# Kernel optimization log

Hardware: AMD Instinct MI355X
Metric: run time of the kernel (lower is better)

The kernel has to match this reference:

```python
import jax, jax.numpy as jnp
import numpy as np

D_MODEL = 1024
D_FF = 4 * D_MODEL
NUM_EXPERTS = 8
TOP_K = 2
BATCH, SEQ = 2, 2048


def setup_inputs() -> dict:
    key = jax.random.key(0)
    ks = jax.random.split(key, 6)
    s_in = 1.0 / np.sqrt(D_MODEL)
    s_ff = 1.0 / np.sqrt(D_FF)
    x = jax.random.normal(ks[0], (BATCH, SEQ, D_MODEL), dtype=jnp.float32)
    Wg = jax.random.uniform(ks[1], (D_MODEL, NUM_EXPERTS), minval=-s_in, maxval=s_in, dtype=jnp.float32)
    W1 = jax.random.uniform(ks[2], (NUM_EXPERTS, D_MODEL, D_FF), minval=-s_in, maxval=s_in, dtype=jnp.float32)
    b1 = jax.random.uniform(ks[3], (NUM_EXPERTS, D_FF), minval=-s_in, maxval=s_in, dtype=jnp.float32)
    W2 = jax.random.uniform(ks[4], (NUM_EXPERTS, D_FF, D_MODEL), minval=-s_ff, maxval=s_ff, dtype=jnp.float32)
    b2 = jax.random.uniform(ks[5], (NUM_EXPERTS, D_MODEL), minval=-s_ff, maxval=s_ff, dtype=jnp.float32)
    return {"x": x, "Wg": Wg, "W1": W1, "b1": b1, "W2": W2, "b2": b2}


def reference(x, Wg, W1, b1, W2, b2):
    B, S, D = x.shape
    x_flat = x.reshape(-1, D)                      # [T, D]
    gate_logits = x_flat @ Wg                      # [T, E] (eval mode: no noise)
    gate_probs = jax.nn.softmax(gate_logits, axis=-1)
    top_v, top_i = jax.lax.top_k(gate_probs, TOP_K)            # [T, k]
    top_v = top_v / (jnp.sum(top_v, axis=-1, keepdims=True) + 1e-8)
    out = jnp.zeros_like(x_flat)
    for e in range(NUM_EXPERTS):
        # combine weight for expert e: sum of normalized top-k probs routed here
        w_e = jnp.sum(jnp.where(top_i == e, top_v, 0.0), axis=-1)   # [T]
        h = jax.nn.gelu(x_flat @ W1[e] + b1[e], approximate=False)  # [T, F]
        y = h @ W2[e] + b2[e]                                       # [T, D]
        out = out + w_e[:, None] * y
    return out.reshape(B, S, D)
```

## Files before the change

### kernel.cpp

```cpp
#include <hip/hip_runtime.h>
#include <math.h>

typedef __attribute__((ext_vector_type(8))) short short8;
typedef __attribute__((ext_vector_type(4))) float f32x4;
typedef unsigned short u16;

#define NT 4096
#define DM 1024
#define DF 4096
#define NE 8
#define HROWS 9216

static __device__ __forceinline__ u16 f2bf(float f) {
  union { float f; unsigned u; } v; v.f = f;
  return (u16)((v.u + 0x7fffu + ((v.u >> 16) & 1u)) >> 16);
}

static __device__ __forceinline__ void gload16(const void* g, void* l) {
  __builtin_amdgcn_global_load_lds((const __attribute__((address_space(1))) void*)g,
                                   (__attribute__((address_space(3))) void*)l, 16, 0, 0);
}

__global__ __launch_bounds__(256) void gate_k(const float* __restrict__ x,
                                              const float* __restrict__ Wg,
                                              int* __restrict__ te,
                                              float* __restrict__ tw) {
  int t = blockIdx.x * 4 + (threadIdx.x >> 6);
  int l = threadIdx.x & 63;
  float a0=0,a1=0,a2=0,a3=0,a4=0,a5=0,a6=0,a7=0;
  const float* xr = x + (size_t)t * DM;
  for (int k = l; k < DM; k += 64) {
    float xv = xr[k];
    const float4* wp = (const float4*)(Wg + k * 8);
    float4 w0 = wp[0], w1 = wp[1];
    a0 += xv * w0.x; a1 += xv * w0.y; a2 += xv * w0.z; a3 += xv * w0.w;
    a4 += xv * w1.x; a5 += xv * w1.y; a6 += xv * w1.z; a7 += xv * w1.w;
  }
#pragma unroll
  for (int s = 32; s >= 1; s >>= 1) {
    a0 += __shfl_down(a0, s); a1 += __shfl_down(a1, s);
    a2 += __shfl_down(a2, s); a3 += __shfl_down(a3, s);
    a4 += __shfl_down(a4, s); a5 += __shfl_down(a5, s);
    a6 += __shfl_down(a6, s); a7 += __shfl_down(a7, s);
  }
  if (l == 0) {
    float lg[8] = {a0,a1,a2,a3,a4,a5,a6,a7};
    float m = lg[0];
#pragma unroll
    for (int e = 1; e < 8; ++e) m = fmaxf(m, lg[e]);
    float p[8], s = 0.f;
#pragma unroll
    for (int e = 0; e < 8; ++e) { p[e] = expf(lg[e] - m); s += p[e]; }
#pragma unroll
    for (int e = 0; e < 8; ++e) p[e] /= s;
    int i0 = 0; float v0 = p[0];
#pragma unroll
    for (int e = 1; e < 8; ++e) if (p[e] > v0) { v0 = p[e]; i0 = e; }
    int i1 = -1; float v1 = -1.f;
#pragma unroll
    for (int e = 0; e < 8; ++e) {
      if (e == i0) continue;
      if (p[e] > v1) { v1 = p[e]; i1 = e; }
    }
    float norm = v0 + v1 + 1e-8f;
    te[t*2]   = i0; te[t*2+1] = i1;
    tw[t*2]   = v0 / norm; tw[t*2+1] = v1 / norm;
  }
}

__global__ __launch_bounds__(256) void route_k(const int* __restrict__ te,
                                               const float* __restrict__ tw,
                                               int* __restrict__ meta,
                                               int* __restrict__ lt,
                                               float* __restrict__ lw) {
  int i = blockIdx.x * 256 + threadIdx.x;
  if (i >= NT * 2) return;
  int e = te[i];
  float w = tw[i];
  int pos = atomicAdd(&meta[e], 1);
  lt[e * NT + pos] = i;
  lw[e * NT + pos] = w;
}

__global__ __launch_bounds__(256) void finalize_k(int* __restrict__ meta,
                                                  int* __restrict__ lt,
                                                  float* __restrict__ lw) {
  __shared__ int s_cnt[8], s_pc[8];
  if (threadIdx.x == 0) {
    int base = 0;
    for (int e = 0; e < 8; ++e) {
      int c = meta[e];
      int pc = (c + 127) & ~127;
      s_cnt[e] = c; s_pc[e] = pc;
      meta[8 + e] = pc;
      meta[16 + e] = base;
      base += pc;
    }
  }
  __syncthreads();
  for (int e = 0; e < 8; ++e) {
    int c = s_cnt[e], pc = s_pc[e];
    for (int i = c + (int)threadIdx.x; i < pc; i += 256) {
      lt[e * NT + i] = 2 * NT;
      lw[e * NT + i] = 0.f;
    }
  }
}

__global__ __launch_bounds__(256) void prep_x(const float* __restrict__ x, u16* __restrict__ xbf) {
  size_t i = (size_t)blockIdx.x * 256 + threadIdx.x;
  const float4* p = (const float4*)(x + i * 8);
  float4 a = p[0], b = p[1];
  short8 o = { (short)f2bf(a.x), (short)f2bf(a.y), (short)f2bf(a.z), (short)f2bf(a.w),
               (short)f2bf(b.x), (short)f2bf(b.y), (short)f2bf(b.z), (short)f2bf(b.w) };
  *(short8*)(xbf + i * 8) = o;
}

__global__ __launch_bounds__(256) void prep_wT(const float* __restrict__ in,
                                               u16* __restrict__ out, int K, int N) {
  const int e = blockIdx.z;
  const int n0 = blockIdx.x * 64, k0 = blockIdx.y * 64;
  const float* ie = in + (size_t)e * K * N;
  u16* oe = out + (size_t)e * K * N;
  __shared__ u16 t[64 * 72];
  const int tid = threadIdx.x;
  const int kr = tid >> 4, nq = (tid & 15) * 4;
#pragma unroll
  for (int it = 0; it < 4; ++it) {
    int k = it * 16 + kr;
    float4 v = *(const float4*)(ie + (size_t)(k0 + k) * N + n0 + nq);
    t[(nq + 0) * 72 + k] = f2bf(v.x);
    t[(nq + 1) * 72 + k] = f2bf(v.y);
    t[(nq + 2) * 72 + k] = f2bf(v.z);
    t[(nq + 3) * 72 + k] = f2bf(v.w);
  }
  __syncthreads();
#pragma unroll
  for (int it = 0; it < 2; ++it) {
    int idx = it * 256 + tid;
    int n = idx >> 3, kc = idx & 7;
    short8 v = *(const short8*)&t[n * 72 + kc * 8];
    *(short8*)(oe + (size_t)(n0 + n) * K + k0 + kc * 8) = v;
  }
}

__global__ __launch_bounds__(256) void ffn1_k(const u16* __restrict__ xbf,
                                              const u16* __restrict__ W1T,
                                              const float* __restrict__ b1,
                                              const int* __restrict__ lt,
                                              const int* __restrict__ meta,
                                              u16* __restrict__ H) {
  const int e = blockIdx.z, mt = blockIdx.y, nt = blockIdx.x;
  const int pc = meta[8 + e];
  if (mt * 128 >= pc) return;
  const int rbase = meta[16 + e];

  __shared__ u16 As[128 * 32];
  __shared__ u16 Bs[128 * 32];

  const int tid = threadIdx.x, lane = tid & 63, wv = tid >> 6;
  const int wm = wv >> 1, wn = wv & 1, l15 = lane & 15, l4 = lane >> 4;

  const u16* pa[2]; const u16* pb[2]; u16* la[2]; u16* lb[2];
#pragma unroll
  for (int it = 0; it < 2; ++it) {
    int idx = it * 256 + tid;
    int r = idx >> 2, s = idx & 3;
    int kg = s ^ ((r >> 1) & 3);
    int tok = lt[e * NT + mt * 128 + r] >> 1;
    if (tok >= NT) tok = 0;
    pa[it] = xbf + (size_t)tok * DM + kg * 8;
    pb[it] = W1T + ((size_t)e * DF + nt * 128 + r) * DM + kg * 8;
    la[it] = As + (it * 256 + wv * 64) * 8;
    lb[it] = Bs + (it * 256 + wv * 64) * 8;
  }

  int aoff[4], boff[4];
#pragma unroll
  for (int i = 0; i < 4; ++i) {
    int ra = wm * 64 + i * 16 + l15;
    aoff[i] = ra * 32 + (l4 ^ ((ra >> 1) & 3)) * 8;
    int rb = wn * 64 + i * 16 + l15;
    boff[i] = rb * 32 + (l4 ^ ((rb >> 1) & 3)) * 8;
  }

  f32x4 acc[4][4];
#pragma unroll
  for (int mi = 0; mi < 4; ++mi)
#pragma unroll
    for (int ni = 0; ni < 4; ++ni) acc[mi][ni] = 0.f;

  for (int ks = 0; ks < DM / 32; ++ks) {
    __syncthreads();
    gload16(pa[0], la[0]); gload16(pa[1], la[1]);
    gload16(pb[0], lb[0]); gload16(pb[1], lb[1]);
    pa[0] += 32; pa[1] += 32; pb[0] += 32; pb[1] += 32;
    __syncthreads();

    short8 af[4], bf_[4];
#pragma unroll
    for (int i = 0; i < 4; ++i) {
      af[i]  = *(const short8*)&As[aoff[i]];
      bf_[i] = *(const short8*)&Bs[boff[i]];
    }
#pragma unroll
    for (int mi = 0; mi < 4; ++mi)
#pragma unroll
      for (int ni = 0; ni < 4; ++ni)
        acc[mi][ni] = __builtin_amdgcn_mfma_f32_16x16x32_bf16(af[mi], bf_[ni], acc[mi][ni], 0, 0, 0);
  }

  const size_t hrow0 = (size_t)rbase + mt * 128;
#pragma unroll
  for (int mi = 0; mi < 4; ++mi) {
#pragma unroll
    for (int ni = 0; ni < 4; ++ni) {
      int gn = nt * 128 + wn * 64 + ni * 16 + l15;
      float bias = b1[e * DF + gn];
      int r0 = wm * 64 + mi * 16 + l4 * 4;
#pragma unroll
      for (int j = 0; j < 4; ++j) {
        float v = acc[mi][ni][j] + bias;
        v = 0.5f * v * (1.0f + erff(v * 0.70710678118654752f));
        H[(hrow0 + r0 + j) * DF + gn] = f2bf(v);
      }
    }
  }
}

template <bool USEY>
__global__ __launch_bounds__(256) void ffn2_k(const u16* __restrict__ H,
                                              const u16* __restrict__ W2T,
                                              const float* __restrict__ b2,
                                              const int* __restrict__ lt,
                                              const float* __restrict__ lw,
                                              const int* __restrict__ meta,
                                              float* __restrict__ Y,
                                              float* __restrict__ out) {
  const int e = blockIdx.z, mt = blockIdx.y, nt = blockIdx.x;
  const int pc = meta[8 + e];
  if (mt * 128 >= pc) return;
  const int rbase = meta[16 + e];

  __shared__ u16 As[128 * 32];
  __shared__ u16 Bs[128 * 32];
  __shared__ int s_ts[128];
  __shared__ float s_w[128];

  const int tid = threadIdx.x, lane = tid & 63, wv = tid >> 6;
  const int wm = wv >> 1, wn = wv & 1, l15 = lane & 15, l4 = lane >> 4;

  if (tid < 128) {
    s_ts[tid] = lt[e * NT + mt * 128 + tid];
    s_w[tid]  = lw[e * NT + mt * 128 + tid];
  }

  const u16* pa[2]; const u16* pb[2]; u16* la[2]; u16* lb[2];
#pragma unroll
  for (int it = 0; it < 2; ++it) {
    int idx = it * 256 + tid;
    int r = idx >> 2, s = idx & 3;
    int kg = s ^ ((r >> 1) & 3);
    pa[it] = H + ((size_t)rbase + mt * 128 + r) * DF + kg * 8;
    pb[it] = W2T + ((size_t)e * DM + nt * 128 + r) * DF + kg * 8;
    la[it] = As + (it * 256 + wv * 64) * 8;
    lb[it] = Bs + (it * 256 + wv * 64) * 8;
  }

  int aoff[4], boff[4];
#pragma unroll
  for (int i = 0; i < 4; ++i) {
    int ra = wm * 64 + i * 16 + l15;
    aoff[i] = ra * 32 + (l4 ^ ((ra >> 1) & 3)) * 8;
    int rb = wn * 64 + i * 16 + l15;
    boff[i] = rb * 32 + (l4 ^ ((rb >> 1) & 3)) * 8;
  }

  f32x4 acc[4][4];
#pragma unroll
  for (int mi = 0; mi < 4; ++mi)
#pragma unroll
    for (int ni = 0; ni < 4; ++ni) acc[mi][ni] = 0.f;

  for (int ks = 0; ks < DF / 32; ++ks) {
    __syncthreads();
    gload16(pa[0], la[0]); gload16(pa[1], la[1]);
    gload16(pb[0], lb[0]); gload16(pb[1], lb[1]);
    pa[0] += 32; pa[1] += 32; pb[0] += 32; pb[1] += 32;
    __syncthreads();

    short8 af[4], bf_[4];
#pragma unroll
    for (int i = 0; i < 4; ++i) {
      af[i]  = *(const short8*)&As[aoff[i]];
      bf_[i] = *(const short8*)&Bs[boff[i]];
    }
#pragma unroll
    for (int mi = 0; mi < 4; ++mi)
#pragma unroll
      for (int ni = 0; ni < 4; ++ni)
        acc[mi][ni] = __builtin_amdgcn_mfma_f32_16x16x32_bf16(af[mi], bf_[ni], acc[mi][ni], 0, 0, 0);
  }

#pragma unroll
  for (int mi = 0; mi < 4; ++mi) {
#pragma unroll
    for (int ni = 0; ni < 4; ++ni) {
      int gn = nt * 128 + wn * 64 + ni * 16 + l15;
      float bias = b2[e * DM + gn];
      int r0 = wm * 64 + mi * 16 + l4 * 4;
#pragma unroll
      for (int j = 0; j < 4; ++j) {
        int r = r0 + j;
        float w = s_w[r];
        int ts = s_ts[r];
        float v = w * (acc[mi][ni][j] + bias);
        if (USEY) {
          Y[(size_t)ts * DM + gn] = v;
        } else {
          int tok = ts >> 1;
          if (tok >= NT) tok = 0;
          atomicAdd(out + (size_t)tok * DM + gn, v);
        }
      }
    }
  }
}

__global__ __launch_bounds__(256) void combine_k(const float* __restrict__ Y,
                                                 float* __restrict__ out) {
  size_t i4 = (size_t)blockIdx.x * 256 + threadIdx.x;
  size_t t = i4 >> 8;
  int c4 = (int)(i4 & 255) * 4;
  const float4 a = *(const float4*)(Y + (2 * t) * DM + c4);
  const float4 b = *(const float4*)(Y + (2 * t + 1) * DM + c4);
  float4 o = { a.x + b.x, a.y + b.y, a.z + b.z, a.w + b.w };
  *(float4*)(out + t * DM + c4) = o;
}

extern "C" void kernel_launch(void* const* d_in, const int* in_sizes, int n_in,
                              void* d_out, int out_size, void* d_ws, size_t ws_size,
                              hipStream_t stream) {
  const float* x  = (const float*)d_in[0];
  const float* Wg = (const float*)d_in[1];
  const float* W1 = (const float*)d_in[2];
  const float* b1 = (const float*)d_in[3];
  const float* W2 = (const float*)d_in[4];
  const float* b2 = (const float*)d_in[5];
  float* out = (float*)d_out;

  char* ws = (char*)d_ws;
  size_t o = 0;
  auto take = [&](size_t sz) { size_t p = o; o = (o + sz + 1023) & ~(size_t)1023; return p; };

  int*   meta = (int*)(ws + take(1024));
  int*   te   = (int*)(ws + take((size_t)NT * 2 * 4));
  float* tw   = (float*)(ws + take((size_t)NT * 2 * 4));
  int*   lt   = (int*)(ws + take((size_t)NE * NT * 4));
  float* lw   = (float*)(ws + take((size_t)NE * NT * 4));
  u16*   xbf  = (u16*)(ws + take((size_t)NT * DM * 2));
  u16*   W1T  = (u16*)(ws + take((size_t)NE * DM * DF * 2));
  u16*   H    = (u16*)(ws + take((size_t)HROWS * DF * 2));
  size_t needB = o;
  size_t needA = needB + ((size_t)NE * DM * DF * 2 + 1024) + ((size_t)(2 * NT + 8) * DM * 4 + 1024);

  bool pathA = (ws_size >= needA);
  u16*   W2T;
  float* Y = nullptr;
  if (pathA) {
    W2T = (u16*)(ws + take((size_t)NE * DM * DF * 2));
    Y   = (float*)(ws + take((size_t)(2 * NT + 8) * DM * 4));
  } else {
    W2T = W1T;
  }

  hipMemsetAsync(meta, 0, 1024, stream);
  if (!pathA) hipMemsetAsync(out, 0, (size_t)NT * DM * 4, stream);

  gate_k<<<NT / 4, 256, 0, stream>>>(x, Wg, te, tw);
  route_k<<<(NT * 2) / 256, 256, 0, stream>>>(te, tw, meta, lt, lw);
  finalize_k<<<1, 256, 0, stream>>>(meta, lt, lw);
  prep_x<<<(NT * DM / 8) / 256, 256, 0, stream>>>(x, xbf);
  prep_wT<<<dim3(DF / 64, DM / 64, NE), 256, 0, stream>>>(W1, W1T, DM, DF);
  if (pathA)
    prep_wT<<<dim3(DM / 64, DF / 64, NE), 256, 0, stream>>>(W2, W2T, DF, DM);

  ffn1_k<<<dim3(DF / 128, NT / 128, NE), 256, 0, stream>>>(xbf, W1T, b1, lt, meta, H);

  if (!pathA)
    prep_wT<<<dim3(DM / 64, DF / 64, NE), 256, 0, stream>>>(W2, W2T, DF, DM);

  if (pathA) {
    ffn2_k<true><<<dim3(DM / 128, NT / 128, NE), 256, 0, stream>>>(H, W2T, b2, lt, lw, meta, Y, out);
    combine_k<<<NT, 256, 0, stream>>>(Y, out);
  } else {
    ffn2_k<false><<<dim3(DM / 128, NT / 128, NE), 256, 0, stream>>>(H, W2T, b2, lt, lw, meta, Y, out);
  }
}
```

Measured before the change: 395.3 us.

## Double-buffer LDS in expert GEMMs, compact tile list, split-K for FFN2

Both expert GEMM kernels now use two LDS buffers. The next K-slice is loaded with global_load_lds while MFMAs run on the current one, and each step ends with one waitcnt and barrier instead of two barriers. The grid is built from a compact list of (expert, m-tile) pairs written by finalize_k, so empty blocks are not launched. When workspace allows, FFN2 splits K into two halves that write separate Y buffers, which combine_k sums. This raises occupancy for the small FFN2 grid at the cost of double LDS use and an extra Y buffer to write and read.

```diff
diff --git a/kernel.cpp b/kernel.cpp
--- a/kernel.cpp
+++ b/kernel.cpp
@@ -10,6 +10,8 @@
 #define DF 4096
 #define NE 8
 #define HROWS 9216
+#define TIT 72
+#define YROWS (2 * NT + 8)
 
 static __device__ __forceinline__ u16 f2bf(float f) {
   union { float f; unsigned u; } v; v.f = f;
@@ -87,7 +89,7 @@
                                                   float* __restrict__ lw) {
   __shared__ int s_cnt[8], s_pc[8];
   if (threadIdx.x == 0) {
-    int base = 0;
+    int base = 0, nt_ = 0;
     for (int e = 0; e < 8; ++e) {
       int c = meta[e];
       int pc = (c + 127) & ~127;
@@ -95,7 +97,9 @@
       meta[8 + e] = pc;
       meta[16 + e] = base;
       base += pc;
-    }
+      for (int mt = 0; mt < pc / 128; ++mt) meta[32 + nt_++] = (e << 16) | mt;
+    }
+    meta[24] = nt_;
   }
   __syncthreads();
   for (int e = 0; e < 8; ++e) {
@@ -144,36 +148,46 @@
   }
 }
 
+#define STAGE4(b)                                            \
+  do {                                                       \
+    gload16(pa0, laA + (b) * 4096 + lda0);                   \
+    gload16(pa1, laA + (b) * 4096 + lda1);                   \
+    gload16(pb0, laB + (b) * 4096 + lda0);                   \
+    gload16(pb1, laB + (b) * 4096 + lda1);                   \
+    pa0 += 32; pa1 += 32; pb0 += 32; pb1 += 32;              \
+  } while (0)
+
 __global__ __launch_bounds__(256) void ffn1_k(const u16* __restrict__ xbf,
                                               const u16* __restrict__ W1T,
                                               const float* __restrict__ b1,
                                               const int* __restrict__ lt,
                                               const int* __restrict__ meta,
                                               u16* __restrict__ H) {
-  const int e = blockIdx.z, mt = blockIdx.y, nt = blockIdx.x;
-  const int pc = meta[8 + e];
-  if (mt * 128 >= pc) return;
+  const int nt = blockIdx.x;
+  const int ti = blockIdx.y;
+  if (ti >= meta[24]) return;
+  const int em = meta[32 + ti];
+  const int e = em >> 16, mt = em & 0xffff;
   const int rbase = meta[16 + e];
 
-  __shared__ u16 As[128 * 32];
-  __shared__ u16 Bs[128 * 32];
+  __shared__ u16 As[2 * 4096];
+  __shared__ u16 Bs[2 * 4096];
 
   const int tid = threadIdx.x, lane = tid & 63, wv = tid >> 6;
   const int wm = wv >> 1, wn = wv & 1, l15 = lane & 15, l4 = lane >> 4;
 
-  const u16* pa[2]; const u16* pb[2]; u16* la[2]; u16* lb[2];
-#pragma unroll
-  for (int it = 0; it < 2; ++it) {
-    int idx = it * 256 + tid;
-    int r = idx >> 2, s = idx & 3;
-    int kg = s ^ ((r >> 1) & 3);
-    int tok = lt[e * NT + mt * 128 + r] >> 1;
-    if (tok >= NT) tok = 0;
-    pa[it] = xbf + (size_t)tok * DM + kg * 8;
-    pb[it] = W1T + ((size_t)e * DF + nt * 128 + r) * DM + kg * 8;
-    la[it] = As + (it * 256 + wv * 64) * 8;
-    lb[it] = Bs + (it * 256 + wv * 64) * 8;
-  }
+  int r0i = tid >> 2, s0 = tid & 3;
+  int r1i = (256 + tid) >> 2, s1 = s0;
+  int kg0 = s0 ^ ((r0i >> 1) & 3);
+  int kg1 = s1 ^ ((r1i >> 1) & 3);
+  int tok0 = lt[e * NT + mt * 128 + r0i] >> 1; if (tok0 >= NT) tok0 = 0;
+  int tok1 = lt[e * NT + mt * 128 + r1i] >> 1; if (tok1 >= NT) tok1 = 0;
+  const u16* pa0 = xbf + (size_t)tok0 * DM + kg0 * 8;
+  const u16* pa1 = xbf + (size_t)tok1 * DM + kg1 * 8;
+  const u16* pb0 = W1T + ((size_t)e * DF + nt * 128 + r0i) * DM + kg0 * 8;
+  const u16* pb1 = W1T + ((size_t)e * DF + nt * 128 + r1i) * DM + kg1 * 8;
+  u16* laA = As; u16* laB = Bs;
+  const int lda0 = (wv * 64) * 8, lda1 = (256 + wv * 64) * 8;
 
   int aoff[4], boff[4];
 #pragma unroll
@@ -190,24 +204,28 @@
 #pragma unroll
     for (int ni = 0; ni < 4; ++ni) acc[mi][ni] = 0.f;
 
-  for (int ks = 0; ks < DM / 32; ++ks) {
-    __syncthreads();
-    gload16(pa[0], la[0]); gload16(pa[1], la[1]);
-    gload16(pb[0], lb[0]); gload16(pb[1], lb[1]);
-    pa[0] += 32; pa[1] += 32; pb[0] += 32; pb[1] += 32;
-    __syncthreads();
-
+  STAGE4(0);
+  asm volatile("s_waitcnt vmcnt(0)" ::: "memory");
+  __builtin_amdgcn_s_barrier();
+
+  const int NK = DM / 32;
+  int cur = 0;
+  for (int ks = 0; ks < NK; ++ks) {
+    if (ks + 1 < NK) STAGE4(cur ^ 1);
     short8 af[4], bf_[4];
 #pragma unroll
     for (int i = 0; i < 4; ++i) {
-      af[i]  = *(const short8*)&As[aoff[i]];
-      bf_[i] = *(const short8*)&Bs[boff[i]];
+      af[i]  = *(const short8*)&As[cur * 4096 + aoff[i]];
+      bf_[i] = *(const short8*)&Bs[cur * 4096 + boff[i]];
     }
 #pragma unroll
     for (int mi = 0; mi < 4; ++mi)
 #pragma unroll
       for (int ni = 0; ni < 4; ++ni)
         acc[mi][ni] = __builtin_amdgcn_mfma_f32_16x16x32_bf16(af[mi], bf_[ni], acc[mi][ni], 0, 0, 0);
+    asm volatile("s_waitcnt vmcnt(0)" ::: "memory");
+    __builtin_amdgcn_s_barrier();
+    cur ^= 1;
   }
 
   const size_t hrow0 = (size_t)rbase + mt * 128;
@@ -217,12 +235,12 @@
     for (int ni = 0; ni < 4; ++ni) {
       int gn = nt * 128 + wn * 64 + ni * 16 + l15;
       float bias = b1[e * DF + gn];
-      int r0 = wm * 64 + mi * 16 + l4 * 4;
+      int rr = wm * 64 + mi * 16 + l4 * 4;
 #pragma unroll
       for (int j = 0; j < 4; ++j) {
         float v = acc[mi][ni][j] + bias;
         v = 0.5f * v * (1.0f + erff(v * 0.70710678118654752f));
-        H[(hrow0 + r0 + j) * DF + gn] = f2bf(v);
+        H[(hrow0 + rr + j) * DF + gn] = f2bf(v);
       }
     }
   }
@@ -237,13 +255,17 @@
                                               const int* __restrict__ meta,
                                               float* __restrict__ Y,
                                               float* __restrict__ out) {
-  const int e = blockIdx.z, mt = blockIdx.y, nt = blockIdx.x;
-  const int pc = meta[8 + e];
-  if (mt * 128 >= pc) return;
+  const int nt = blockIdx.x;
+  const int ti = blockIdx.y;
+  if (ti >= meta[24]) return;
+  const int kz = blockIdx.z, nz = gridDim.z;
+  const int em = meta[32 + ti];
+  const int e = em >> 16, mt = em & 0xffff;
   const int rbase = meta[16 + e];
-
-  __shared__ u16 As[128 * 32];
-  __shared__ u16 Bs[128 * 32];
+  const int KLEN = DF / nz, KOFF = kz * KLEN;
+
+  __shared__ u16 As[2 * 4096];
+  __shared__ u16 Bs[2 * 4096];
   __shared__ int s_ts[128];
   __shared__ float s_w[128];
 
@@ -255,17 +277,16 @@
     s_w[tid]  = lw[e * NT + mt * 128 + tid];
   }
 
-  const u16* pa[2]; const u16* pb[2]; u16* la[2]; u16* lb[2];
-#pragma unroll
-  for (int it = 0; it < 2; ++it) {
-    int idx = it * 256 + tid;
-    int r = idx >> 2, s = idx & 3;
-    int kg = s ^ ((r >> 1) & 3);
-    pa[it] = H + ((size_t)rbase + mt * 128 + r) * DF + kg * 8;
-    pb[it] = W2T + ((size_t)e * DM + nt * 128 + r) * DF + kg * 8;
-    la[it] = As + (it * 256 + wv * 64) * 8;
-    lb[it] = Bs + (it * 256 + wv * 64) * 8;
-  }
+  int r0i = tid >> 2, s0 = tid & 3;
+  int r1i = (256 + tid) >> 2;
+  int kg0 = s0 ^ ((r0i >> 1) & 3);
+  int kg1 = s0 ^ ((r1i >> 1) & 3);
+  const u16* pa0 = H + ((size_t)rbase + mt * 128 + r0i) * DF + KOFF + kg0 * 8;
+  const u16* pa1 = H + ((size_t)rbase + mt * 128 + r1i) * DF + KOFF + kg1 * 8;
+  const u16* pb0 = W2T + ((size_t)e * DM + nt * 128 + r0i) * DF + KOFF + kg0 * 8;
+  const u16* pb1 = W2T + ((size_t)e * DM + nt * 128 + r1i) * DF + KOFF + kg1 * 8;
+  u16* laA = As; u16* laB = Bs;
+  const int lda0 = (wv * 64) * 8, lda1 = (256 + wv * 64) * 8;
 
   int aoff[4], boff[4];
 #pragma unroll
@@ -282,24 +303,28 @@
 #pragma unroll
     for (int ni = 0; ni < 4; ++ni) acc[mi][ni] = 0.f;
 
-  for (int ks = 0; ks < DF / 32; ++ks) {
-    __syncthreads();
-    gload16(pa[0], la[0]); gload16(pa[1], la[1]);
-    gload16(pb[0], lb[0]); gload16(pb[1], lb[1]);
-    pa[0] += 32; pa[1] += 32; pb[0] += 32; pb[1] += 32;
-    __syncthreads();
-
+  STAGE4(0);
+  asm volatile("s_waitcnt vmcnt(0)" ::: "memory");
+  __builtin_amdgcn_s_barrier();
+
+  const int NK = KLEN / 32;
+  int cur = 0;
+  for (int ks = 0; ks < NK; ++ks) {
+    if (ks + 1 < NK) STAGE4(cur ^ 1);
     short8 af[4], bf_[4];
 #pragma unroll
     for (int i = 0; i < 4; ++i) {
-      af[i]  = *(const short8*)&As[aoff[i]];
-      bf_[i] = *(const short8*)&Bs[boff[i]];
+      af[i]  = *(const short8*)&As[cur * 4096 + aoff[i]];
+      bf_[i] = *(const short8*)&Bs[cur * 4096 + boff[i]];
     }
 #pragma unroll
     for (int mi = 0; mi < 4; ++mi)
 #pragma unroll
       for (int ni = 0; ni < 4; ++ni)
         acc[mi][ni] = __builtin_amdgcn_mfma_f32_16x16x32_bf16(af[mi], bf_[ni], acc[mi][ni], 0, 0, 0);
+    asm volatile("s_waitcnt vmcnt(0)" ::: "memory");
+    __builtin_amdgcn_s_barrier();
+    cur ^= 1;
   }
 
 #pragma unroll
@@ -307,16 +332,16 @@
 #pragma unroll
     for (int ni = 0; ni < 4; ++ni) {
       int gn = nt * 128 + wn * 64 + ni * 16 + l15;
-      float bias = b2[e * DM + gn];
-      int r0 = wm * 64 + mi * 16 + l4 * 4;
+      float bias = (kz == 0) ? b2[e * DM + gn] : 0.f;
+      int rr = wm * 64 + mi * 16 + l4 * 4;
 #pragma unroll
       for (int j = 0; j < 4; ++j) {
-        int r = r0 + j;
+        int r = rr + j;
         float w = s_w[r];
         int ts = s_ts[r];
         float v = w * (acc[mi][ni][j] + bias);
         if (USEY) {
-          Y[(size_t)ts * DM + gn] = v;
+          Y[((size_t)kz * YROWS + ts) * DM + gn] = v;
         } else {
           int tok = ts >> 1;
           if (tok >= NT) tok = 0;
@@ -328,13 +353,18 @@
 }
 
 __global__ __launch_bounds__(256) void combine_k(const float* __restrict__ Y,
-                                                 float* __restrict__ out) {
+                                                 float* __restrict__ out, int nz) {
   size_t i4 = (size_t)blockIdx.x * 256 + threadIdx.x;
   size_t t = i4 >> 8;
   int c4 = (int)(i4 & 255) * 4;
   const float4 a = *(const float4*)(Y + (2 * t) * DM + c4);
   const float4 b = *(const float4*)(Y + (2 * t + 1) * DM + c4);
   float4 o = { a.x + b.x, a.y + b.y, a.z + b.z, a.w + b.w };
+  if (nz == 2) {
+    const float4 c = *(const float4*)(Y + ((size_t)YROWS + 2 * t) * DM + c4);
+    const float4 d = *(const float4*)(Y + ((size_t)YROWS + 2 * t + 1) * DM + c4);
+    o.x += c.x + d.x; o.y += c.y + d.y; o.z += c.z + d.z; o.w += c.w + d.w;
+  }
   *(float4*)(out + t * DM + c4) = o;
 }
 
@@ -362,38 +392,40 @@
   u16*   W1T  = (u16*)(ws + take((size_t)NE * DM * DF * 2));
   u16*   H    = (u16*)(ws + take((size_t)HROWS * DF * 2));
   size_t needB = o;
-  size_t needA = needB + ((size_t)NE * DM * DF * 2 + 1024) + ((size_t)(2 * NT + 8) * DM * 4 + 1024);
-
-  bool pathA = (ws_size >= needA);
+  size_t ySz = (size_t)YROWS * DM * 4;
+  size_t needA  = needB + ((size_t)NE * DM * DF * 2 + 1024) + (ySz + 1024);
+  size_t needA2 = needA + ySz + 1024;
+
+  int nz = (ws_size >= needA2) ? 2 : (ws_size >= needA ? 1 : 0);
   u16*   W2T;
   float* Y = nullptr;
-  if (pathA) {
+  if (nz > 0) {
     W2T = (u16*)(ws + take((size_t)NE * DM * DF * 2));
-    Y   = (float*)(ws + take((size_t)(2 * NT + 8) * DM * 4));
+    Y   = (float*)(ws + take((size_t)nz * ySz));
   } else {
     W2T = W1T;
   }
 
   hipMemsetAsync(meta, 0, 1024, stream);
-  if (!pathA) hipMemsetAsync(out, 0, (size_t)NT * DM * 4, stream);
+  if (nz == 0) hipMemsetAsync(out, 0, (size_t)NT * DM * 4, stream);
 
   gate_k<<<NT / 4, 256, 0, stream>>>(x, Wg, te, tw);
   route_k<<<(NT * 2) / 256, 256, 0, stream>>>(te, tw, meta, lt, lw);
   finalize_k<<<1, 256, 0, stream>>>(meta, lt, lw);
   prep_x<<<(NT * DM / 8) / 256, 256, 0, stream>>>(x, xbf);
   prep_wT<<<dim3(DF / 64, DM / 64, NE), 256, 0, stream>>>(W1, W1T, DM, DF);
-  if (pathA)
+  if (nz > 0)
     prep_wT<<<dim3(DM / 64, DF / 64, NE), 256, 0, stream>>>(W2, W2T, DF, DM);
 
-  ffn1_k<<<dim3(DF / 128, NT / 128, NE), 256, 0, stream>>>(xbf, W1T, b1, lt, meta, H);
-
-  if (!pathA)
+  ffn1_k<<<dim3(DF / 128, TIT), 256, 0, stream>>>(xbf, W1T, b1, lt, meta, H);
+
+  if (nz == 0)
     prep_wT<<<dim3(DM / 64, DF / 64, NE), 256, 0, stream>>>(W2, W2T, DF, DM);
 
-  if (pathA) {
-    ffn2_k<true><<<dim3(DM / 128, NT / 128, NE), 256, 0, stream>>>(H, W2T, b2, lt, lw, meta, Y, out);
-    combine_k<<<NT, 256, 0, stream>>>(Y, out);
+  if (nz > 0) {
+    ffn2_k<true><<<dim3(DM / 128, TIT, nz), 256, 0, stream>>>(H, W2T, b2, lt, lw, meta, Y, out);
+    combine_k<<<NT, 256, 0, stream>>>(Y, out, nz);
   } else {
-    ffn2_k<false><<<dim3(DM / 128, NT / 128, NE), 256, 0, stream>>>(H, W2T, b2, lt, lw, meta, Y, out);
-  }
-}
+    ffn2_k<false><<<dim3(DM / 128, TIT, 1), 256, 0, stream>>>(H, W2T, b2, lt, lw, meta, Y, out);
+  }
+}
```

Measured after the change: 420.2 us. 1.06x slower.
